# Kernel optimization log

Measured on AMD Instinct MI355X. Metric: run time of the kernel, lower is better.

The kernel has to match this reference:

```python
import jax, jax.numpy as jnp
import numpy as np


def _rotate_every_two(x):
    # interleaved pairs: (x0, x1) -> (-x1, x0)
    x1 = x[..., ::2]
    x2 = x[..., 1::2]
    return jnp.stack((-x2, x1), axis=-1).reshape(x.shape)


def setup_inputs() -> dict:
    key = jax.random.key(0)
    ks = jax.random.split(key, 6)
    B, S, D = 2, 2048, 1024
    w = lambda k, shape: jax.random.normal(k, shape, dtype=jnp.float32) * 0.02
    return {
        "x": jax.random.normal(ks[0], (B, S, D), dtype=jnp.float32),
        "Wq": w(ks[1], (D, D)), "bq": jnp.zeros((D,), jnp.float32),
        "Wk": w(ks[2], (D, D)), "bk": jnp.zeros((D,), jnp.float32),
        "Wv": w(ks[3], (D, 2 * D)), "bv": jnp.zeros((2 * D,), jnp.float32),
        "Wg": w(ks[4], (D, 2 * D)), "bg": jnp.zeros((2 * D,), jnp.float32),
        "Wo": w(ks[5], (2 * D, D)), "bo": jnp.zeros((D,), jnp.float32),
    }


def reference(x, Wq, bq, Wk, bk, Wv, bv, Wg, bg, Wo, bo):
    B, S, D = x.shape
    H = 16
    key_dim = D // H          # 64
    head_dim = 2 * D // H     # 128 (factor=2)
    scaling = key_dim ** -0.5

    # RetNetRelPos buffers (deterministic)
    angle = 1.0 / 10000.0 ** jnp.linspace(0.0, 1.0, key_dim // 2)
    angle = jnp.repeat(angle, 2).astype(jnp.float32)          # [key_dim]
    decay = jnp.log(1.0 - 2.0 ** (-5.0 - jnp.arange(H, dtype=jnp.float32)))  # [H]

    idx = jnp.arange(S, dtype=jnp.float32)
    sin = jnp.sin(idx[:, None] * angle[None, :])              # [S, key_dim]
    cos = jnp.cos(idx[:, None] * angle[None, :])

    # causal exponential decay mask, normalized by sqrt(rowsum)
    diff = idx[:, None] - idx[None, :]                        # [S, S]
    mask = jnp.where(diff >= 0, jnp.exp(decay[:, None, None] * diff), 0.0)  # [H,S,S]
    mask = mask / jnp.sqrt(mask.sum(-1, keepdims=True))

    q = (x @ Wq + bq).reshape(B, S, H, key_dim).transpose(0, 2, 1, 3)              # [B,H,S,kd]
    k = ((x @ Wk + bk) * scaling).reshape(B, S, H, key_dim).transpose(0, 2, 1, 3)
    v = x @ Wv + bv                                                                # [B,S,2D]
    g = x @ Wg + bg

    qr = q * cos + _rotate_every_two(q) * sin
    kr = k * cos + _rotate_every_two(k) * sin
    vr = v.reshape(B, S, H, head_dim).transpose(0, 2, 1, 3)                        # [B,H,S,hd]

    qk = jnp.einsum('bhsd,bhtd->bhst', qr, kr) * mask                              # [B,H,S,S]
    denom = jnp.clip(jnp.abs(jax.lax.stop_gradient(qk).sum(-1, keepdims=True)), 1.0, None)
    qk = qk / denom

    out = jnp.einsum('bhst,bhtd->bhsd', qk, vr).transpose(0, 2, 1, 3)              # [B,S,H,hd]

    # LayerNorm over head_dim, eps=1e-5, no affine (biased variance as in torch)
    mu = out.mean(-1, keepdims=True)
    var = ((out - mu) ** 2).mean(-1, keepdims=True)
    out = (out - mu) / jnp.sqrt(var + 1e-5)

    out = out.reshape(B, S, H * head_dim)                                          # [B,S,2D]
    out = jax.nn.silu(g) * out
    return out @ Wo + bo
```

## Files before the change

### kernel.cpp

```cpp
#include <hip/hip_runtime.h>
#include <hip/hip_bf16.h>

typedef __attribute__((ext_vector_type(8))) unsigned short ushort8;
typedef __attribute__((ext_vector_type(4))) float f32x4;
typedef __attribute__((ext_vector_type(8))) __bf16 bf16x8;
typedef unsigned int u32_g __attribute__((address_space(1)));
typedef unsigned int u32_l __attribute__((address_space(3)));

__device__ __forceinline__ float bf2f(unsigned short u) {
  union { unsigned u; float f; } v; v.u = ((unsigned)u) << 16; return v.f;
}
__device__ __forceinline__ unsigned short f2bf(float f) {
  union { float f; unsigned u; } v; v.f = f;
  unsigned r = v.u + 0x7FFFu + ((v.u >> 16) & 1u);
  return (unsigned short)(r >> 16);
}
__device__ __forceinline__ unsigned cvtpk_bf16(float lo, float hi) {
  unsigned r;
  asm("v_cvt_pk_bf16_f32 %0, %1, %2" : "=v"(r) : "v"(lo), "v"(hi));
  return r;
}
__device__ __forceinline__ f32x4 mfma16(bf16x8 a, bf16x8 b, f32x4 c) {
  return __builtin_amdgcn_mfma_f32_16x16x32_bf16(a, b, c, 0, 0, 0);
}
__device__ __forceinline__ void gload16(const void* g, void* l) {
  __builtin_amdgcn_global_load_lds((const u32_g*)g, (u32_l*)l, 16, 0, 0);
}

__device__ __forceinline__ void tc_body(
    const float* __restrict__ W, unsigned short* __restrict__ WT,
    int K, int N, int ldwt, int row_off, int bx, int by, int tid,
    unsigned short* t)
{
  int n0 = bx * 64, k0 = by * 64;
#pragma unroll
  for (int i = 0; i < 4; i++) {
    int c = tid + 256 * i;
    int r = c >> 4, q = c & 15;
    float4 v = *(const float4*)&W[(size_t)(k0 + r) * N + n0 + q * 4];
    t[(q * 4 + 0) * 80 + r] = f2bf(v.x);
    t[(q * 4 + 1) * 80 + r] = f2bf(v.y);
    t[(q * 4 + 2) * 80 + r] = f2bf(v.z);
    t[(q * 4 + 3) * 80 + r] = f2bf(v.w);
  }
  __syncthreads();
#pragma unroll
  for (int i = 0; i < 2; i++) {
    int c = tid + 256 * i;
    int n = c >> 3, p = c & 7;
    *(ushort8*)&WT[(size_t)(row_off + n0 + n) * ldwt + k0 + p * 8] =
        *(const ushort8*)&t[n * 80 + p * 8];
  }
}

__global__ __launch_bounds__(256) void mega_prep_kernel(
    const float* __restrict__ x,
    const float* __restrict__ Wq, const float* __restrict__ Wk,
    const float* __restrict__ Wv, const float* __restrict__ Wg,
    const float* __restrict__ Wo,
    const float* __restrict__ bq, const float* __restrict__ bk,
    const float* __restrict__ bv, const float* __restrict__ bg,
    unsigned short* __restrict__ wcatT, unsigned short* __restrict__ woT,
    unsigned short* __restrict__ xbf, float* __restrict__ bcat)
{
  __shared__ unsigned short t[64 * 80];
  int bid = blockIdx.x, tid = threadIdx.x;
  if (bid < 256) {
    tc_body(Wq, wcatT, 1024, 1024, 1024, 0, bid & 15, bid >> 4, tid, t);
  } else if (bid < 512) {
    int l = bid - 256;
    tc_body(Wk, wcatT, 1024, 1024, 1024, 1024, l & 15, l >> 4, tid, t);
  } else if (bid < 1024) {
    int l = bid - 512;
    tc_body(Wv, wcatT, 1024, 2048, 1024, 2048, l & 31, l >> 5, tid, t);
  } else if (bid < 1536) {
    int l = bid - 1024;
    tc_body(Wg, wcatT, 1024, 2048, 1024, 4096, l & 31, l >> 5, tid, t);
  } else if (bid < 2048) {
    int l = bid - 1536;
    tc_body(Wo, woT, 2048, 1024, 2048, 0, l & 15, l >> 4, tid, t);
  } else if (bid < 6144) {
    size_t i = (size_t)((bid - 2048) * 256 + tid) * 4;
    float4 v = *(const float4*)&x[i];
    unsigned r0 = (unsigned)f2bf(v.x) | ((unsigned)f2bf(v.y) << 16);
    unsigned r1 = (unsigned)f2bf(v.z) | ((unsigned)f2bf(v.w) << 16);
    uint2 o; o.x = r0; o.y = r1;
    *(uint2*)&xbf[i] = o;
  } else {
    int i = (bid - 6144) * 256 + tid;
    float v;
    if (i < 1024) v = bq[i];
    else if (i < 2048) v = bk[i - 1024];
    else if (i < 4096) v = bv[i - 2048];
    else v = bg[i - 4096];
    bcat[i] = v;
  }
}

template<int OUT_BF16, int BN, int SM, int SN>
__global__ __launch_bounds__(256, 3) void gemm3_kernel(
    const unsigned short* __restrict__ A, const unsigned short* __restrict__ BT,
    const float* __restrict__ bias, void* __restrict__ Cout,
    int M, int N, int K)
{
  constexpr int BUFS = (128 + BN) * 32;
  constexpr int ACH  = 512;
  constexpr int LPS  = (128 + BN) / 64;
  constexpr int STB  = SM * SN;
  __shared__ __attribute__((aligned(16))) unsigned short lds[3 * BUFS];
  int tid = threadIdx.x, wave = tid >> 6, lane = tid & 63;
  int lr = lane & 15, lg = lane >> 4;
  int gx = gridDim.x;
  int lin = blockIdx.x + gx * blockIdx.y;
  int cpx = (gx * gridDim.y) >> 3;
  int xcd = lin & 7, s = lin >> 3;
  int spx = cpx / STB;
  int sup = xcd * spx + s / STB;
  int nSupN = gx / SN;
  int stm = sup / nSupN, stn = sup % nSupN;
  int idx = s % STB;
  int m0 = (stm * SM + idx / SN) * 128;
  int n0 = (stn * SN + idx % SN) * BN;
  int wr = (wave >> 1) * 64, wc = (wave & 1) * (BN / 2);
  constexpr int NR = BN / 32;

  const unsigned short* gsrc[LPS];
#pragma unroll
  for (int i = 0; i < LPS; i++) {
    int c = tid + i * 256;
    if (c < ACH) {
      int r = c >> 2, j = c & 3;
      gsrc[i] = A + (size_t)(m0 + r) * K + ((j ^ ((r >> 1) & 3)) << 3);
    } else {
      int c2 = c - ACH, r = c2 >> 2, j = c2 & 3;
      gsrc[i] = BT + (size_t)(n0 + r) * K + ((j ^ ((r >> 1) & 3)) << 3);
    }
  }

  auto stage = [&](int buf, int kt) {
    char* lb = (char*)(lds + buf * BUFS);
#pragma unroll
    for (int i = 0; i < LPS; i++)
      gload16(gsrc[i] + kt * 32, lb + (tid + i * 256) * 16);
  };

  f32x4 acc[4][NR] = {};
  int nk = K >> 5;
  stage(0, 0);
  stage(1, 1);
  int cb = 0;
  for (int it = 0; it < nk; it++) {
    if (it + 1 < nk) {
      if constexpr (LPS == 4) asm volatile("s_waitcnt vmcnt(4)" ::: "memory");
      else                    asm volatile("s_waitcnt vmcnt(3)" ::: "memory");
    } else {
      asm volatile("s_waitcnt vmcnt(0)" ::: "memory");
    }
    __builtin_amdgcn_sched_barrier(0);
    __builtin_amdgcn_s_barrier();
    __builtin_amdgcn_sched_barrier(0);
    if (it + 2 < nk) {
      int sb = cb + 2; if (sb >= 3) sb -= 3;
      stage(sb, it + 2);
    }
    const unsigned short* as = lds + cb * BUFS;
    const unsigned short* bs = as + 128 * 32;
    int csw = (lg ^ ((lr >> 1) & 3)) << 3;
    bf16x8 af[4], bfr[NR];
#pragma unroll
    for (int m = 0; m < 4; m++)
      af[m] = *(const bf16x8*)&as[(wr + m * 16 + lr) * 32 + csw];
#pragma unroll
    for (int n = 0; n < NR; n++)
      bfr[n] = *(const bf16x8*)&bs[(wc + n * 16 + lr) * 32 + csw];
    __builtin_amdgcn_s_setprio(1);
#pragma unroll
    for (int m = 0; m < 4; m++)
#pragma unroll
      for (int n = 0; n < NR; n++)
        acc[m][n] = mfma16(af[m], bfr[n], acc[m][n]);
    __builtin_amdgcn_s_setprio(0);
    cb++; if (cb == 3) cb = 0;
  }

#pragma unroll
  for (int m = 0; m < 4; m++) {
#pragma unroll
    for (int n = 0; n < NR; n++) {
      int col = n0 + wc + n * 16 + lr;
      float bv = bias ? bias[col] : 0.f;
#pragma unroll
      for (int r = 0; r < 4; r++) {
        int row = m0 + wr + m * 16 + lg * 4 + r;
        float v = acc[m][n][r] + bv;
        if (OUT_BF16)
          ((unsigned short*)Cout)[(size_t)row * N + col] = f2bf(v);
        else
          ((float*)Cout)[(size_t)row * N + col] = v;
      }
    }
  }
}

__global__ __launch_bounds__(256) void prep2_kernel(
    const unsigned short* __restrict__ Y,
    unsigned short* __restrict__ qr, unsigned short* __restrict__ kr,
    unsigned short* __restrict__ vT)
{
  int bid = blockIdx.x, tid = threadIdx.x;
  if (bid < 8192) {
    int t = bid * 256 + tid;
    int j = t & 31;
    int h = (t >> 5) & 15;
    int bs = t >> 9;
    int s = bs & 2047;
    int b = bs >> 11;
    float ang = __expf(-0.29710774f * (float)j);
    float th = (float)s * ang;
    float sn, cs;
    __sincosf(th, &sn, &cs);
    const unsigned short* yq = &Y[(size_t)bs * 6144 + h * 64 + 2 * j];
    unsigned qv = *(const unsigned*)yq;
    unsigned kv = *(const unsigned*)(yq + 1024);
    float q0 = bf2f((unsigned short)(qv & 0xffff));
    float q1 = bf2f((unsigned short)(qv >> 16));
    float k0 = bf2f((unsigned short)(kv & 0xffff)) * 0.125f;
    float k1 = bf2f((unsigned short)(kv >> 16)) * 0.125f;
    float qr0 = q0 * cs - q1 * sn, qr1 = q1 * cs + q0 * sn;
    float kr0 = k0 * cs - k1 * sn, kr1 = k1 * cs + k0 * sn;
    size_t o = ((size_t)(b * 16 + h) * 2048 + s) * 64 + 2 * j;
    *(unsigned*)&qr[o] = (unsigned)f2bf(qr0) | ((unsigned)f2bf(qr1) << 16);
    *(unsigned*)&kr[o] = (unsigned)f2bf(kr0) | ((unsigned)f2bf(kr1) << 16);
  } else {
    __shared__ unsigned short t[128 * 80];
    int l = bid - 8192;
    int s0 = (l & 31) * 64;
    int bh = l >> 5;
    int b = bh >> 4, h = bh & 15;
#pragma unroll
    for (int i = 0; i < 4; i++) {
      int c = tid + 256 * i;
      int r = c >> 4, p = c & 15;
      ushort8 v = *(const ushort8*)&Y[(size_t)(b * 2048 + s0 + r) * 6144 + 2048 + h * 128 + p * 8];
#pragma unroll
      for (int e = 0; e < 8; e++) t[(p * 8 + e) * 80 + r] = v[e];
    }
    __syncthreads();
#pragma unroll
    for (int i = 0; i < 4; i++) {
      int c = tid + 256 * i;
      int d = c >> 3, p = c & 7;
      *(ushort8*)&vT[((size_t)bh * 128 + d) * 2048 + s0 + p * 8] = *(const ushort8*)&t[d * 80 + p * 8];
    }
  }
}

#define LPAD 72
__global__ __launch_bounds__(256, 2) void retention_kernel(
    const unsigned short* __restrict__ qr, const unsigned short* __restrict__ kr,
    const unsigned short* __restrict__ vT, const unsigned short* __restrict__ Yg,
    unsigned short* __restrict__ Z)
{
  __shared__ __attribute__((aligned(16))) unsigned short lds[24576 + 4 * 16 * LPAD];
  unsigned short* const lk0 = lds;
  unsigned short* const lk1 = lds + 4096;
  unsigned short* const lv0 = lds + 8192;
  unsigned short* const lv1 = lds + 16384;
  unsigned short* const lp  = lds + 24576;

  int lin = blockIdx.x;
  int xcd = lin & 7, slot = lin >> 3;
  int bh = xcd + 8 * (slot >> 4);
  int bx = slot & 15;
  int b = bh >> 4, h = bh & 15;
  float decay = __logf(1.f - exp2f(-5.f - (float)h));
  int tid = threadIdx.x, wave = tid >> 6, lane = tid & 63;
  int lr = lane & 15, lg = lane >> 4;
  const unsigned short* qbase = &qr[(size_t)bh * 2048 * 64];
  const unsigned short* kbase = &kr[(size_t)bh * 2048 * 64];
  const unsigned short* vbase = &vT[(size_t)bh * 128 * 2048];
  unsigned short* lpw = &lp[wave * 16 * LPAD];
  int swz = (lr & 7) << 3;

  float cf[4][4];
#pragma unroll
  for (int nb = 0; nb < 4; nb++)
#pragma unroll
    for (int r = 0; r < 4; r++)
      cf[nb][r] = __expf(-decay * (float)(nb * 16 + lg * 4 + r));

  auto stage = [&](int bufi, int t0) {
    const char* kg = (const char*)(kbase + (size_t)t0 * 64);
    const char* vg = (const char*)vbase + (size_t)t0 * 2;
    char* lk = (char*)(bufi ? lk1 : lk0);
    char* lv = (char*)(bufi ? lv1 : lv0);
#pragma unroll
    for (int i = 0; i < 2; i++) {
      int c = tid + i * 256;
      int r = c >> 3, j = c & 7;
      gload16(kg + r * 128 + ((j ^ (r & 7)) << 4), lk + c * 16);
    }
#pragma unroll
    for (int i = 0; i < 4; i++) {
      int c = tid + i * 256;
      int d = c >> 3, j = c & 7;
      gload16(vg + (size_t)d * 4096 + ((j ^ (d & 7)) << 4), lv + c * 16);
    }
  };

  for (int pass = 0; pass < 2; pass++) {
    int stile = pass ? 31 - bx : bx;
    int s0 = stile * 64;
    int sq = s0 + wave * 16 + lr;
    bf16x8 qf0 = *(const bf16x8*)&qbase[(size_t)sq * 64 + lg * 8];
    bf16x8 qf1 = *(const bf16x8*)&qbase[(size_t)sq * 64 + 32 + lg * 8];
    f32x4 accv[8] = {};
    float rs = 0.f;
    int nt = stile + 1;

    stage(0, 0);
    __syncthreads();
    for (int it = 0; it < nt; it++) {
      int t0 = it * 64;
      if (it + 1 < nt) stage((it + 1) & 1, t0 + 64);
      const unsigned short* lk = (it & 1) ? lk1 : lk0;
      const unsigned short* lv = (it & 1) ? lv1 : lv0;
      bool bnd = (it == nt - 1);
      float rowf = __expf(decay * (float)(sq - t0));
#pragma unroll
      for (int nb = 0; nb < 4; nb++) {
        f32x4 sa = {};
        bf16x8 a0 = *(const bf16x8*)&lk[((nb * 16 + lr) * 64 + lg * 8) ^ swz];
        bf16x8 a1 = *(const bf16x8*)&lk[((nb * 16 + lr) * 64 + 32 + lg * 8) ^ swz];
        __builtin_amdgcn_s_setprio(1);
        sa = mfma16(a0, qf0, sa);
        sa = mfma16(a1, qf1, sa);
        __builtin_amdgcn_s_setprio(0);
        float pv[4];
#pragma unroll
        for (int r = 0; r < 4; r++) {
          float w = rowf * cf[nb][r];
          if (bnd) {
            int tt = t0 + nb * 16 + lg * 4 + r;
            w = (tt <= sq) ? w : 0.f;
          }
          pv[r] = sa[r] * w;
          rs += pv[r];
        }
        uint2 wv;
        wv.x = cvtpk_bf16(pv[0], pv[1]);
        wv.y = cvtpk_bf16(pv[2], pv[3]);
        *(uint2*)&lpw[lr * LPAD + nb * 16 + lg * 4] = wv;
      }
      __builtin_amdgcn_s_setprio(1);
#pragma unroll
      for (int kk = 0; kk < 2; kk++) {
        bf16x8 pa = *(const bf16x8*)&lpw[lr * LPAD + kk * 32 + lg * 8];
#pragma unroll
        for (int nb = 0; nb < 8; nb++) {
          bf16x8 bv = *(const bf16x8*)&lv[((nb * 16 + lr) * 64 + kk * 32 + lg * 8) ^ swz];
          accv[nb] = mfma16(pa, bv, accv[nb]);
        }
      }
      __builtin_amdgcn_s_setprio(0);
      __syncthreads();
    }

    rs += __shfl_xor(rs, 16);
    rs += __shfl_xor(rs, 32);
    int srb = s0 + wave * 16 + lg * 4;
    const unsigned short* gb2 = &Yg[((size_t)(b * 2048 + srb)) * 6144 + 4096 + h * 128];
    unsigned short* zb = &Z[((size_t)(b * 2048 + srb)) * 2048 + h * 128];
#pragma unroll
    for (int r = 0; r < 4; r++) {
      float rsq = __shfl(rs, lg * 4 + r);
      float sidx = (float)(srb + r);
      float geo = (1.f - __expf(decay * (sidx + 1.f))) * exp2f(5.f + (float)h);
      float invs = rsqrtf(geo);
      float den = fmaxf(fabsf(rsq * invs), 1.f);
      float scl = invs / den;
      float sm = 0.f, sq2 = 0.f;
#pragma unroll
      for (int nb = 0; nb < 8; nb++) {
        float v = accv[nb][r] * scl;
        sm += v; sq2 += v * v;
      }
      sm += __shfl_xor(sm, 1); sm += __shfl_xor(sm, 2);
      sm += __shfl_xor(sm, 4); sm += __shfl_xor(sm, 8);
      sq2 += __shfl_xor(sq2, 1); sq2 += __shfl_xor(sq2, 2);
      sq2 += __shfl_xor(sq2, 4); sq2 += __shfl_xor(sq2, 8);
      float mu = sm * (1.f / 128.f);
      float var = sq2 * (1.f / 128.f) - mu * mu;
      float istd = rsqrtf(var + 1e-5f);
#pragma unroll
      for (int nb = 0; nb < 8; nb++) {
        float v = accv[nb][r] * scl;
        float nrm = (v - mu) * istd;
        float g = bf2f(gb2[(size_t)r * 6144 + nb * 16 + lr]);
        float sg = g / (1.f + __expf(-g));
        zb[(size_t)r * 2048 + nb * 16 + lr] = f2bf(nrm * sg);
      }
    }
  }
}

extern "C" void kernel_launch(void* const* d_in, const int* in_sizes, int n_in,
                              void* d_out, int out_size, void* d_ws, size_t ws_size,
                              hipStream_t stream) {
  const float* x  = (const float*)d_in[0];
  const float* Wq = (const float*)d_in[1];
  const float* bq = (const float*)d_in[2];
  const float* Wk = (const float*)d_in[3];
  const float* bk = (const float*)d_in[4];
  const float* Wv = (const float*)d_in[5];
  const float* bv = (const float*)d_in[6];
  const float* Wg = (const float*)d_in[7];
  const float* bg = (const float*)d_in[8];
  const float* Wo = (const float*)d_in[9];
  const float* bo = (const float*)d_in[10];

  char* ws = (char*)d_ws;
  unsigned short* xbf   = (unsigned short*)(ws);
  unsigned short* wcatT = (unsigned short*)(ws + 8388608);
  unsigned short* woT   = (unsigned short*)(ws + 20971520);
  unsigned short* Y     = (unsigned short*)(ws + 25165824);
  unsigned short* qrb   = (unsigned short*)(ws + 75497472);
  unsigned short* krb   = (unsigned short*)(ws + 83886080);
  unsigned short* vT    = (unsigned short*)(ws + 92274688);
  float*          bcat  = (float*)(ws + 109051904);
  unsigned short* Z     = xbf;

  mega_prep_kernel<<<6168, 256, 0, stream>>>(x, Wq, Wk, Wv, Wg, Wo,
                                             bq, bk, bv, bg,
                                             wcatT, woT, xbf, bcat);

  gemm3_kernel<1, 128, 8, 6><<<dim3(48, 32), 256, 0, stream>>>(xbf, wcatT, bcat, Y, 4096, 6144, 1024);

  prep2_kernel<<<9216, 256, 0, stream>>>(Y, qrb, krb, vT);

  retention_kernel<<<512, 256, 0, stream>>>(qrb, krb, vT, Y, Z);

  gemm3_kernel<0, 64, 4, 4><<<dim3(16, 32), 256, 0, stream>>>(Z, woT, bo, d_out, 4096, 1024, 2048);
}
```

Measured before the change: 183.3 us.

## Fuse RoPE and V transpose into QKVG projection GEMM epilogue

Removes the separate prep2 kernel by applying rotary embedding to q/k, k scaling, and the V transpose directly in the projection GEMM epilogue. Q and K are written in head-major layout, V is written transposed, and only G still goes to Y. This saves the Y round trip through memory for q/k/v and one kernel launch. In exchange the epilogue does scattered, poorly coalesced stores, and the swizzle grouping changes from 8x6 to 4x4.

After: 161.2 us. 1.14x faster.

```diff
diff --git a/kernel.cpp b/kernel.cpp
--- a/kernel.cpp
+++ b/kernel.cpp
@@ -97,10 +97,12 @@
   }
 }
 
-template<int OUT_BF16, int BN, int SM, int SN>
+template<int OUT_MODE, int BN, int SM, int SN>
 __global__ __launch_bounds__(256, 3) void gemm3_kernel(
     const unsigned short* __restrict__ A, const unsigned short* __restrict__ BT,
     const float* __restrict__ bias, void* __restrict__ Cout,
+    unsigned short* __restrict__ qout, unsigned short* __restrict__ kout,
+    unsigned short* __restrict__ vout, unsigned short* __restrict__ gout,
     int M, int N, int K)
 {
   constexpr int BUFS = (128 + BN) * 32;
@@ -183,74 +185,77 @@
     cb++; if (cb == 3) cb = 0;
   }
 
-#pragma unroll
-  for (int m = 0; m < 4; m++) {
-#pragma unroll
-    for (int n = 0; n < NR; n++) {
-      int col = n0 + wc + n * 16 + lr;
-      float bv = bias ? bias[col] : 0.f;
-#pragma unroll
-      for (int r = 0; r < 4; r++) {
-        int row = m0 + wr + m * 16 + lg * 4 + r;
-        float v = acc[m][n][r] + bv;
-        if (OUT_BF16)
-          ((unsigned short*)Cout)[(size_t)row * N + col] = f2bf(v);
-        else
-          ((float*)Cout)[(size_t)row * N + col] = v;
-      }
-    }
-  }
-}
-
-__global__ __launch_bounds__(256) void prep2_kernel(
-    const unsigned short* __restrict__ Y,
-    unsigned short* __restrict__ qr, unsigned short* __restrict__ kr,
-    unsigned short* __restrict__ vT)
-{
-  int bid = blockIdx.x, tid = threadIdx.x;
-  if (bid < 8192) {
-    int t = bid * 256 + tid;
-    int j = t & 31;
-    int h = (t >> 5) & 15;
-    int bs = t >> 9;
-    int s = bs & 2047;
-    int b = bs >> 11;
-    float ang = __expf(-0.29710774f * (float)j);
-    float th = (float)s * ang;
-    float sn, cs;
-    __sincosf(th, &sn, &cs);
-    const unsigned short* yq = &Y[(size_t)bs * 6144 + h * 64 + 2 * j];
-    unsigned qv = *(const unsigned*)yq;
-    unsigned kv = *(const unsigned*)(yq + 1024);
-    float q0 = bf2f((unsigned short)(qv & 0xffff));
-    float q1 = bf2f((unsigned short)(qv >> 16));
-    float k0 = bf2f((unsigned short)(kv & 0xffff)) * 0.125f;
-    float k1 = bf2f((unsigned short)(kv >> 16)) * 0.125f;
-    float qr0 = q0 * cs - q1 * sn, qr1 = q1 * cs + q0 * sn;
-    float kr0 = k0 * cs - k1 * sn, kr1 = k1 * cs + k0 * sn;
-    size_t o = ((size_t)(b * 16 + h) * 2048 + s) * 64 + 2 * j;
-    *(unsigned*)&qr[o] = (unsigned)f2bf(qr0) | ((unsigned)f2bf(qr1) << 16);
-    *(unsigned*)&kr[o] = (unsigned)f2bf(kr0) | ((unsigned)f2bf(kr1) << 16);
+  if constexpr (OUT_MODE == 0) {
+#pragma unroll
+    for (int m = 0; m < 4; m++) {
+#pragma unroll
+      for (int n = 0; n < NR; n++) {
+        int col = n0 + wc + n * 16 + lr;
+        float bv = bias ? bias[col] : 0.f;
+#pragma unroll
+        for (int r = 0; r < 4; r++) {
+          int row = m0 + wr + m * 16 + lg * 4 + r;
+          ((float*)Cout)[(size_t)row * N + col] = acc[m][n][r] + bv;
+        }
+      }
+    }
   } else {
-    __shared__ unsigned short t[128 * 80];
-    int l = bid - 8192;
-    int s0 = (l & 31) * 64;
-    int bh = l >> 5;
-    int b = bh >> 4, h = bh & 15;
-#pragma unroll
-    for (int i = 0; i < 4; i++) {
-      int c = tid + 256 * i;
-      int r = c >> 4, p = c & 15;
-      ushort8 v = *(const ushort8*)&Y[(size_t)(b * 2048 + s0 + r) * 6144 + 2048 + h * 128 + p * 8];
-#pragma unroll
-      for (int e = 0; e < 8; e++) t[(p * 8 + e) * 80 + r] = v[e];
-    }
-    __syncthreads();
-#pragma unroll
-    for (int i = 0; i < 4; i++) {
-      int c = tid + 256 * i;
-      int d = c >> 3, p = c & 7;
-      *(ushort8*)&vT[((size_t)bh * 128 + d) * 2048 + s0 + p * 8] = *(const ushort8*)&t[d * 80 + p * 8];
+    int b = m0 >> 11;
+    if (n0 < 2048) {
+      const bool isk = (n0 >= 1024);
+      unsigned short* dst = isk ? kout : qout;
+      float kscale = isk ? 0.125f : 1.0f;
+#pragma unroll
+      for (int m = 0; m < 4; m++) {
+#pragma unroll
+        for (int n = 0; n < NR; n++) {
+          int col = n0 + wc + n * 16 + lr;
+          int cc = col & 63, hh = (col & 1023) >> 6;
+          float ang = __expf(-0.29710774f * (float)(cc >> 1));
+          float bv = bias[col];
+          int odd = col & 1;
+#pragma unroll
+          for (int r = 0; r < 4; r++) {
+            int row = m0 + wr + m * 16 + lg * 4 + r;
+            float v = acc[m][n][r] + bv;
+            float p = __shfl_xor(v, 1);
+            float sn, cs;
+            __sincosf((float)(row & 2047) * ang, &sn, &cs);
+            float out = odd ? (v * cs + p * sn) : (v * cs - p * sn);
+            dst[((size_t)(b * 16 + hh) * 2048 + (row & 2047)) * 64 + cc] =
+                f2bf(out * kscale);
+          }
+        }
+      }
+    } else if (n0 < 4096) {
+#pragma unroll
+      for (int m = 0; m < 4; m++) {
+#pragma unroll
+        for (int n = 0; n < NR; n++) {
+          int col = n0 + wc + n * 16 + lr;
+          int vcol = col - 2048, hh = vcol >> 7, d = vcol & 127;
+          float bv = bias[col];
+          int s0 = (m0 + wr + m * 16 + lg * 4) & 2047;
+          uint2 wv;
+          wv.x = (unsigned)f2bf(acc[m][n][0] + bv) | ((unsigned)f2bf(acc[m][n][1] + bv) << 16);
+          wv.y = (unsigned)f2bf(acc[m][n][2] + bv) | ((unsigned)f2bf(acc[m][n][3] + bv) << 16);
+          *(uint2*)&vout[((size_t)(b * 16 + hh) * 128 + d) * 2048 + s0] = wv;
+        }
+      }
+    } else {
+#pragma unroll
+      for (int m = 0; m < 4; m++) {
+#pragma unroll
+        for (int n = 0; n < NR; n++) {
+          int col = n0 + wc + n * 16 + lr;
+          float bv = bias[col];
+#pragma unroll
+          for (int r = 0; r < 4; r++) {
+            int row = m0 + wr + m * 16 + lg * 4 + r;
+            gout[(size_t)row * 6144 + col] = f2bf(acc[m][n][r] + bv);
+          }
+        }
+      }
     }
   }
 }
@@ -434,11 +439,11 @@
                                              bq, bk, bv, bg,
                                              wcatT, woT, xbf, bcat);
 
-  gemm3_kernel<1, 128, 8, 6><<<dim3(48, 32), 256, 0, stream>>>(xbf, wcatT, bcat, Y, 4096, 6144, 1024);
-
-  prep2_kernel<<<9216, 256, 0, stream>>>(Y, qrb, krb, vT);
+  gemm3_kernel<1, 128, 4, 4><<<dim3(48, 32), 256, 0, stream>>>(
+      xbf, wcatT, bcat, nullptr, qrb, krb, vT, Y, 4096, 6144, 1024);
 
   retention_kernel<<<512, 256, 0, stream>>>(qrb, krb, vT, Y, Z);
 
-  gemm3_kernel<0, 64, 4, 4><<<dim3(16, 32), 256, 0, stream>>>(Z, woT, bo, d_out, 4096, 1024, 2048);
-}
+  gemm3_kernel<0, 64, 4, 4><<<dim3(16, 32), 256, 0, stream>>>(
+      Z, woT, bo, d_out, nullptr, nullptr, nullptr, nullptr, 4096, 1024, 2048);
+}
```
